# Performance work log

Measured on AMD Instinct MI355X. Metric: run time of the kernel, lower is better.

Reference implementation:

```python
import jax, jax.numpy as jnp
import numpy as np

B, L, H, N2, NLAYERS = 8, 4096, 256, 32, 4


def setup_inputs() -> dict:
    key = jax.random.key(0)
    ks = jax.random.split(key, 7)
    x = jax.random.normal(ks[0], (B, L, H), dtype=jnp.float32)
    # S4D kernel params (per layer, stacked on leading dim)
    dt_min, dt_max = 1e-3, 1e-1
    u = jax.random.uniform(ks[1], (NLAYERS, H), dtype=jnp.float32)
    log_dt = u * (np.log(dt_max) - np.log(dt_min)) + np.log(dt_min)
    log_A_real = jnp.log(0.5 * jnp.ones((NLAYERS, H, N2), jnp.float32))
    A_imag = jnp.broadcast_to(np.pi * jnp.arange(N2, dtype=jnp.float32), (NLAYERS, H, N2)) * jnp.ones((NLAYERS, H, N2), jnp.float32)
    C_re = jax.random.normal(ks[2], (NLAYERS, H, N2), dtype=jnp.float32) * (0.5 ** 0.5)
    C_im = jax.random.normal(ks[3], (NLAYERS, H, N2), dtype=jnp.float32) * (0.5 ** 0.5)
    D = jax.random.normal(ks[4], (NLAYERS, H), dtype=jnp.float32)
    Wout = jax.random.normal(ks[5], (NLAYERS, 2 * H, H), dtype=jnp.float32) * (1.0 / H) ** 0.5
    bout = jnp.zeros((NLAYERS, 2 * H), jnp.float32)
    ln_g = jnp.ones((NLAYERS, H), jnp.float32)
    ln_b = jnp.zeros((NLAYERS, H), jnp.float32)
    return dict(x=x, log_dt=log_dt, log_A_real=log_A_real, A_imag=A_imag,
                C_re=C_re, C_im=C_im, D=D, Wout=Wout, bout=bout,
                ln_g=ln_g, ln_b=ln_b)


def _s4d_kernel(log_dt, log_A_real, A_imag, C_re, C_im, Lseq):
    # Vandermonde kernel of S4D: k[h,l] = 2*Re sum_n C'_hn exp(dt_h*A_hn*l)
    dt = jnp.exp(log_dt)                       # (H,)
    A = (-jnp.exp(log_A_real) + 1j * A_imag)   # (H,N) complex
    C = C_re + 1j * C_im                       # (H,N)
    dtA = A * dt[:, None]                      # (H,N)
    K = jnp.exp(dtA[:, :, None] * jnp.arange(Lseq, dtype=jnp.float32))  # (H,N,L)
    Cm = C * (jnp.exp(dtA) - 1.0) / A          # ZOH discretization of C
    return 2.0 * jnp.einsum('hn,hnl->hl', Cm, K).real  # (H,L)


def _s4d_layer(u, log_dt, log_A_real, A_imag, C_re, C_im, D, Wout, bout):
    # u: (B,H,L)
    Lq = u.shape[-1]
    k = _s4d_kernel(log_dt, log_A_real, A_imag, C_re, C_im, Lq)  # (H,L)
    kf = jnp.fft.rfft(k, n=2 * Lq)             # (H, L+1)
    uf = jnp.fft.rfft(u, n=2 * Lq)             # (B,H,L+1)
    y = jnp.fft.irfft(uf * kf, n=2 * Lq)[..., :Lq]
    y = y + u * D[:, None]
    y = jax.nn.gelu(y, approximate=False)
    # output linear: 1x1 conv H->2H followed by GLU along channel dim
    y = jnp.einsum('oh,bhl->bol', Wout, y) + bout[None, :, None]
    a, b = jnp.split(y, 2, axis=1)
    return a * jax.nn.sigmoid(b)               # (B,H,L)


def _layernorm_ch(x, g, b, eps=1e-5):
    # x: (B,H,L); normalize over channel axis H (matches norm on (B,L,H))
    m = jnp.mean(x, axis=1, keepdims=True)
    v = jnp.mean((x - m) ** 2, axis=1, keepdims=True)
    return (x - m) / jnp.sqrt(v + eps) * g[None, :, None] + b[None, :, None]


def reference(x, log_dt, log_A_real, A_imag, C_re, C_im, D, Wout, bout, ln_g, ln_b):
    u = jnp.swapaxes(x, -1, -2)  # (B,H,L)
    for i in range(NLAYERS):  # post-norm (prenorm=False), dropout=identity (eval)
        z = _s4d_layer(u, log_dt[i], log_A_real[i], A_imag[i], C_re[i], C_im[i],
                       D[i], Wout[i], bout[i])
        u = z + u
        u = _layernorm_ch(u, ln_g[i], ln_b[i])
    return jnp.swapaxes(u, -1, -2)  # (B,L,H)
```

## Files before the change

### kernel.cpp

```cpp
#include <hip/hip_runtime.h>
#include <math.h>

#define B    8
#define L    4096
#define H    256
#define N2   32
#define NL   4
#define O2   512
#define BLK  64
#define NBLK 64
#define TVP  136
#define MJP  72
#define UTP  72
#define INP  66
#define TL2  64
#define YPAD 264

typedef __attribute__((ext_vector_type(8))) short short8;
typedef __attribute__((ext_vector_type(4))) float f32x4;

__device__ __forceinline__ unsigned short f2bf(float f)
{
    unsigned int u = __float_as_uint(f);
    unsigned int r = (u + 0x7fffu + ((u >> 16) & 1u)) >> 16;
    return (unsigned short)r;
}

__device__ __forceinline__ float bf2f(unsigned short v)
{
    return __uint_as_float(((unsigned int)v) << 16);
}

__device__ __forceinline__ float gelu_f(float x)
{
    float t = 1.59576912161f * fmaf(0.044715f * x * x, x, x);
    return x / (1.f + __expf(-t));
}

__global__ __launch_bounds__(64) void k_mats(
    const float* __restrict__ log_dt, const float* __restrict__ log_Ar,
    const float* __restrict__ A_im, const float* __restrict__ C_re,
    const float* __restrict__ C_im, const float* __restrict__ Dv,
    unsigned short* __restrict__ TVc, unsigned short* __restrict__ Mm,
    float2* __restrict__ w64c)
{
    __shared__ float kb[2][BLK];
    const int t = threadIdx.x;
    const int g = t >> 5, n = t & 31;
    const int id = blockIdx.x * 2 + g;
    const int layer = id >> 8, h = id & 255;
    const int idx = (layer * H + h) * N2 + n;
    double dt = exp((double)log_dt[layer * H + h]);
    double Ar = -exp((double)log_Ar[idx]);
    double Ai = (double)A_im[idx];
    double dtr = dt * Ar, dti = dt * Ai;
    double er = exp(dtr);
    double dwr = er * cos(dti), dwi = er * sin(dti);
    double numr = dwr - 1.0, numi = dwi;
    double den = Ar * Ar + Ai * Ai;
    double qr0 = (numr * Ar + numi * Ai) / den;
    double qi0 = (numi * Ar - numr * Ai) / den;
    double dcr = (double)C_re[idx], dci = (double)C_im[idx];
    const float wr = (float)dwr, wi = (float)dwi;
    const float cr = (float)(2.0 * (dcr * qr0 - dci * qi0));
    const float ci = (float)(2.0 * (dcr * qi0 + dci * qr0));
    const float Dh = Dv[layer * H + h];
    unsigned short* tv = TVc + (size_t)(layer * H + h) * BLK * TVP;
    unsigned short* mm = Mm + (size_t)(layer * H + h) * BLK * MJP;
    float vr = 1.f, vi = 0.f;
    for (int d = 0; d < BLK; ++d) {
        float pk = fmaf(cr, vr, -(ci * vi));
        pk += __shfl_xor(pk, 1);  pk += __shfl_xor(pk, 2);
        pk += __shfl_xor(pk, 4);  pk += __shfl_xor(pk, 8);
        pk += __shfl_xor(pk, 16);
        if (n == 0) kb[g][d] = pk;
        mm[n * MJP + (63 - d)]        = f2bf(vr);
        mm[(32 + n) * MJP + (63 - d)] = f2bf(vi);
        float nvr = vr * wr - vi * wi;
        float nvi = vr * wi + vi * wr;
        vr = nvr; vi = nvi;
        float qr = fmaf(cr, vr, -(ci * vi));
        float qi = fmaf(cr, vi, ci * vr);
        tv[d * TVP + 64 + n] = f2bf(qr);
        tv[d * TVP + 96 + n] = f2bf(-qi);
    }
    w64c[(layer * H + h) * N2 + n] = make_float2(vr, vi);
    __syncthreads();
    for (int i = 0; i < BLK; ++i) {
#pragma unroll
        for (int hf = 0; hf < 2; ++hf) {
            int j = n + hf * 32;
            float val = (j > i) ? 0.f : ((j == i) ? (kb[g][0] + Dh) : kb[g][i - j]);
            tv[i * TVP + j] = f2bf(val);
        }
    }
}

__global__ __launch_bounds__(256) void k_tr_xu(const float* __restrict__ x, unsigned short* __restrict__ u)
{
    __shared__ float t[32][33];
    int b = blockIdx.z;
    int h0 = blockIdx.x * 32, l0 = blockIdx.y * 32;
    int tx = threadIdx.x & 31, ty = threadIdx.x >> 5;
    const float* xb = x + (size_t)b * L * H;
    unsigned short* ub = u + (size_t)b * H * L;
#pragma unroll
    for (int i = 0; i < 4; ++i)
        t[ty + i * 8][tx] = xb[(size_t)(l0 + ty + i * 8) * H + h0 + tx];
    __syncthreads();
#pragma unroll
    for (int i = 0; i < 4; ++i)
        ub[(size_t)(h0 + ty + i * 8) * L + l0 + tx] = f2bf(t[tx][ty + i * 8]);
}

__global__ __launch_bounds__(256) void k_wcvt(const float* __restrict__ w, unsigned short* __restrict__ wb)
{
    int idx = (blockIdx.x * 256 + threadIdx.x) * 4;
    float4 v = *(const float4*)(w + idx);
    ushort4 o;
    o.x = f2bf(v.x); o.y = f2bf(v.y); o.z = f2bf(v.z); o.w = f2bf(v.w);
    *(ushort4*)(wb + idx) = o;
}

__global__ __launch_bounds__(256) void k_scan3(
    const unsigned short* __restrict__ u, const unsigned short* __restrict__ Mm_l,
    const unsigned short* __restrict__ TVc_l, const float2* __restrict__ w64c_l,
    unsigned short* __restrict__ y)
{
    __shared__ __align__(16) unsigned short uT[BLK * UTP];
    __shared__ __align__(16) unsigned short ST[BLK * UTP];
    __shared__ float INC[BLK * INP];
    __shared__ float2 cLd[4][32];
    const int t = threadIdx.x;
    const int wv = t >> 6, lane = t & 63;
    const int lanei = lane & 15, quad = lane >> 4;
    const int h = blockIdx.x >> 3, ct = blockIdx.x & 7;
    const unsigned short* ub = u + (size_t)(ct * H + h) * L;

    {
        int col = t >> 2, q = t & 3;
        *(short8*)&uT[col * UTP + q * 16]     = *(const short8*)(ub + col * 64 + q * 16);
        *(short8*)&uT[col * UTP + q * 16 + 8] = *(const short8*)(ub + col * 64 + q * 16 + 8);
    }
    __syncthreads();

    {
        f32x4 acc[4];
#pragma unroll
        for (int nt = 0; nt < 4; ++nt) acc[nt] = (f32x4){0.f, 0.f, 0.f, 0.f};
        const unsigned short* arow = Mm_l + (size_t)h * BLK * MJP + (wv * 16 + lanei) * MJP + quad * 8;
#pragma unroll
        for (int kt = 0; kt < 2; ++kt) {
            short8 a8 = *(const short8*)(arow + kt * 32);
#pragma unroll
            for (int nt = 0; nt < 4; ++nt) {
                short8 b8 = *(const short8*)&uT[(nt * 16 + lanei) * UTP + kt * 32 + quad * 8];
                acc[nt] = __builtin_amdgcn_mfma_f32_16x16x32_bf16(a8, b8, acc[nt], 0, 0, 0);
            }
        }
#pragma unroll
        for (int nt = 0; nt < 4; ++nt) {
            int col = nt * 16 + lanei;
            int k0 = wv * 16 + quad * 4;
#pragma unroll
            for (int reg = 0; reg < 4; ++reg)
                INC[col * INP + k0 + reg] = acc[nt][reg];
        }
    }
    __syncthreads();

    {
        const int n = lane & 31;
        float Pr[16], Pi[16];
        float w1r = 1.f, w1i = 0.f;
        float2 w64 = make_float2(0.f, 0.f);
        if (lane < 32) {
            w64 = w64c_l[h * N2 + n];
            float sr = 0.f, si = 0.f;
            const int base = wv * 16;
#pragma unroll
            for (int k = 0; k < 16; ++k) {
                Pr[k] = sr; Pi[k] = si;
                float ir = INC[(base + k) * INP + n];
                float ii = INC[(base + k) * INP + 32 + n];
                float nr = fmaf(w64.x, sr, fmaf(-w64.y, si, ir));
                float ni = fmaf(w64.x, si, fmaf(w64.y, sr, ii));
                sr = nr; si = ni;
            }
            cLd[wv][n] = make_float2(sr, si);
            float ar = w64.x, ai = w64.y;
#pragma unroll
            for (int q = 0; q < 4; ++q) {
                float nr2 = ar * ar - ai * ai;
                float ni2 = 2.f * ar * ai;
                ar = nr2; ai = ni2;
            }
            w1r = ar; w1i = ai;
        }
        __syncthreads();
        if (lane < 32) {
            float Cr = 0.f, Ci = 0.f;
            for (int wp = 0; wp < wv; ++wp) {
                float2 Lw = cLd[wp][n];
                float nr = fmaf(w1r, Cr, fmaf(-w1i, Ci, Lw.x));
                float ni = fmaf(w1r, Ci, fmaf(w1i, Cr, Lw.y));
                Cr = nr; Ci = ni;
            }
            float pr = 1.f, pi = 0.f;
#pragma unroll
            for (int k = 0; k < 16; ++k) {
                int blk = wv * 16 + k;
                float Sr = fmaf(pr, Cr, fmaf(-pi, Ci, Pr[k]));
                float Si = fmaf(pr, Ci, fmaf(pi, Cr, Pi[k]));
                ST[blk * UTP + n]      = f2bf(Sr);
                ST[blk * UTP + 32 + n] = f2bf(Si);
                float npr = pr * w64.x - pi * w64.y;
                float npi = pr * w64.y + pi * w64.x;
                pr = npr; pi = npi;
            }
        }
    }
    __syncthreads();

    {
        f32x4 acc[4];
#pragma unroll
        for (int nt = 0; nt < 4; ++nt) acc[nt] = (f32x4){0.f, 0.f, 0.f, 0.f};
        const unsigned short* arow = TVc_l + (size_t)h * BLK * TVP + (wv * 16 + lanei) * TVP + quad * 8;
#pragma unroll
        for (int kt = 0; kt < 4; ++kt) {
            short8 a8 = *(const short8*)(arow + kt * 32);
            const unsigned short* bb = (kt < 2) ? uT : ST;
            int ko = (kt & 1) * 32 + quad * 8;
#pragma unroll
            for (int nt = 0; nt < 4; ++nt) {
                short8 b8 = *(const short8*)&bb[(nt * 16 + lanei) * UTP + ko];
                acc[nt] = __builtin_amdgcn_mfma_f32_16x16x32_bf16(a8, b8, acc[nt], 0, 0, 0);
            }
        }
        unsigned short* yb = y + (size_t)(ct * H + h) * L;
#pragma unroll
        for (int nt = 0; nt < 4; ++nt) {
            int blk = nt * 16 + lanei;
            int i0 = wv * 16 + quad * 4;
            ushort4 o4;
            o4.x = f2bf(gelu_f(acc[nt][0]));
            o4.y = f2bf(gelu_f(acc[nt][1]));
            o4.z = f2bf(gelu_f(acc[nt][2]));
            o4.w = f2bf(gelu_f(acc[nt][3]));
            *(ushort4*)(yb + blk * 64 + i0) = o4;
        }
    }
}

__global__ __launch_bounds__(512, 4) void k_gemm(
    const unsigned short* __restrict__ y, unsigned short* __restrict__ u,
    const unsigned short* __restrict__ Wb, const float* __restrict__ bo,
    const float* __restrict__ lng, const float* __restrict__ lnb,
    float* __restrict__ outp)
{
    __shared__ __align__(16) unsigned short yS[TL2 * YPAD];
    __shared__ float bS[O2];
    __shared__ float lgS[H], lbS[H];
    __shared__ float redS[8][4][16], redQ[8][4][16];

    const int t = threadIdx.x;
    const int wv = t >> 6;
    const int lane = t & 63;
    const int lanei = lane & 15;
    const int quad = lane >> 4;
    const int b = blockIdx.x >> 6;
    const int l0 = (blockIdx.x & 63) * TL2;

    {
        const int i = t & 7, hr = t >> 3;
        const unsigned short* yb = y + (size_t)b * H * L + l0 + i * 8;
#pragma unroll
        for (int ps = 0; ps < 4; ++ps) {
            int h = ps * 64 + hr;
            short8 v8 = *(const short8*)(yb + (size_t)h * L);
#pragma unroll
            for (int r = 0; r < 8; ++r)
                yS[(i * 8 + r) * YPAD + (h ^ (8 * i))] = (unsigned short)v8[r];
        }
        if (t < O2) bS[t] = bo[t];
        if (t < H) { lgS[t] = lng[t]; lbS[t] = lnb[t]; }
    }
    __syncthreads();

    f32x4 acc[2][2][4];
#pragma unroll
    for (int p = 0; p < 2; ++p)
#pragma unroll
        for (int jj = 0; jj < 2; ++jj)
#pragma unroll
            for (int nt = 0; nt < 4; ++nt)
                acc[p][jj][nt] = (f32x4){0.f, 0.f, 0.f, 0.f};

    size_t abase[2][2];
#pragma unroll
    for (int p = 0; p < 2; ++p)
#pragma unroll
        for (int jj = 0; jj < 2; ++jj)
            abase[p][jj] = (size_t)(p * 256 + wv * 32 + jj * 16 + lanei) * H + quad * 8;

#pragma unroll
    for (int kt = 0; kt < 8; ++kt) {
        short8 bfr[4];
#pragma unroll
        for (int nt = 0; nt < 4; ++nt) {
            int lp = nt * 16 + lanei;
            int a = (2 * nt + (lanei >> 3)) & 7;
            bfr[nt] = *(const short8*)&yS[lp * YPAD + ((kt * 32 + quad * 8) ^ (8 * a))];
        }
#pragma unroll
        for (int p = 0; p < 2; ++p)
#pragma unroll
            for (int jj = 0; jj < 2; ++jj) {
                short8 a8 = *(const short8*)(Wb + abase[p][jj] + kt * 32);
#pragma unroll
                for (int nt = 0; nt < 4; ++nt)
                    acc[p][jj][nt] = __builtin_amdgcn_mfma_f32_16x16x32_bf16(
                        a8, bfr[nt], acc[p][jj][nt], 0, 0, 0);
            }
    }

    float psum[4] = {0.f, 0.f, 0.f, 0.f}, psq[4] = {0.f, 0.f, 0.f, 0.f};
    unsigned short* ub = u + (size_t)b * H * L + l0;
#pragma unroll
    for (int jj = 0; jj < 2; ++jj) {
#pragma unroll
        for (int nt = 0; nt < 4; ++nt) {
            int lc = nt * 16 + lanei;
#pragma unroll
            for (int reg = 0; reg < 4; ++reg) {
                int o = wv * 32 + jj * 16 + quad * 4 + reg;
                float a = acc[0][jj][nt][reg] + bS[o];
                float g = acc[1][jj][nt][reg] + bS[o + 256];
                float glu = a / (1.f + __expf(-g));
                float val = glu + bf2f(ub[(size_t)o * L + lc]);
                acc[0][jj][nt][reg] = val;
                psum[nt] += val;
                psq[nt] = fmaf(val, val, psq[nt]);
            }
        }
    }
#pragma unroll
    for (int nt = 0; nt < 4; ++nt) {
        psum[nt] += __shfl_xor(psum[nt], 16);
        psum[nt] += __shfl_xor(psum[nt], 32);
        psq[nt]  += __shfl_xor(psq[nt], 16);
        psq[nt]  += __shfl_xor(psq[nt], 32);
    }
    if (lane < 16) {
#pragma unroll
        for (int nt = 0; nt < 4; ++nt) {
            redS[wv][nt][lanei] = psum[nt];
            redQ[wv][nt][lanei] = psq[nt];
        }
    }
    __syncthreads();
    float mcol[4], icol[4];
#pragma unroll
    for (int nt = 0; nt < 4; ++nt) {
        float s = 0.f, q = 0.f;
#pragma unroll
        for (int w = 0; w < 8; ++w) { s += redS[w][nt][lanei]; q += redQ[w][nt][lanei]; }
        float m = s * (1.0f / 256.0f);
        float v = q * (1.0f / 256.0f) - m * m;
        mcol[nt] = m;
        icol[nt] = rsqrtf(v + 1e-5f);
    }
    if (outp == nullptr) {
#pragma unroll
        for (int jj = 0; jj < 2; ++jj) {
#pragma unroll
            for (int nt = 0; nt < 4; ++nt) {
                int lc = nt * 16 + lanei;
#pragma unroll
                for (int reg = 0; reg < 4; ++reg) {
                    int o = wv * 32 + jj * 16 + quad * 4 + reg;
                    float val = acc[0][jj][nt][reg];
                    float ov = (val - mcol[nt]) * icol[nt] * lgS[o] + lbS[o];
                    ub[(size_t)o * L + lc] = f2bf(ov);
                }
            }
        }
    } else {
#pragma unroll
        for (int jj = 0; jj < 2; ++jj) {
#pragma unroll
            for (int nt = 0; nt < 4; ++nt) {
                int lc = nt * 16 + lanei;
                int o0 = wv * 32 + jj * 16 + quad * 4;
                float4 ov;
#pragma unroll
                for (int reg = 0; reg < 4; ++reg) {
                    int o = o0 + reg;
                    float val = acc[0][jj][nt][reg];
                    ((float*)&ov)[reg] = (val - mcol[nt]) * icol[nt] * lgS[o] + lbS[o];
                }
                *(float4*)(outp + ((size_t)b * L + l0 + lc) * H + o0) = ov;
            }
        }
    }
}

extern "C" void kernel_launch(void* const* d_in, const int* in_sizes, int n_in,
                              void* d_out, int out_size, void* d_ws, size_t ws_size,
                              hipStream_t stream)
{
    const float* x      = (const float*)d_in[0];
    const float* log_dt = (const float*)d_in[1];
    const float* log_Ar = (const float*)d_in[2];
    const float* A_im   = (const float*)d_in[3];
    const float* C_re   = (const float*)d_in[4];
    const float* C_im   = (const float*)d_in[5];
    const float* Dv     = (const float*)d_in[6];
    const float* Wout   = (const float*)d_in[7];
    const float* bout   = (const float*)d_in[8];
    const float* lng    = (const float*)d_in[9];
    const float* lnb    = (const float*)d_in[10];
    float* out = (float*)d_out;

    unsigned short* u   = (unsigned short*)d_ws;
    unsigned short* Wb  = u + (size_t)B * H * L;
    unsigned short* TVc = Wb + (size_t)NL * O2 * H;
    unsigned short* Mm  = TVc + (size_t)NL * H * BLK * TVP;
    float2* w64c        = (float2*)(Mm + (size_t)NL * H * BLK * MJP);
    unsigned short* y   = (unsigned short*)(w64c + (size_t)NL * H * N2);

    k_wcvt<<<NL * O2 * H / 1024, 256, 0, stream>>>(Wout, Wb);
    k_mats<<<NL * H / 2, 64, 0, stream>>>(log_dt, log_Ar, A_im, C_re, C_im, Dv, TVc, Mm, w64c);
    k_tr_xu<<<dim3(8, 128, B), 256, 0, stream>>>(x, u);
    for (int layer = 0; layer < NL; ++layer) {
        k_scan3<<<H * 8, 256, 0, stream>>>(u, Mm + (size_t)layer * H * BLK * MJP,
                                           TVc + (size_t)layer * H * BLK * TVP,
                                           w64c + (size_t)layer * H * N2, y);
        k_gemm<<<B * L / TL2, 512, 0, stream>>>(y, u, Wb + (size_t)layer * O2 * H,
                                                bout + layer * O2, lng + layer * H, lnb + layer * H,
                                                (layer == NL - 1) ? out : nullptr);
    }
}
```

Baseline: 321.4 us.

## Swap scan MFMA operands to drop barriers, merge setup kernels, prefetch GEMM weights

In k_scan3 the MFMA operands are swapped so each wave produces and consumes only its own 16 block rows. This lets the INC stores become 16-byte vector writes and removes two block-wide __syncthreads, since the scan and the second GEMM now read only data written by the same wave. The three setup kernels (weight conversion, S4D matrix construction, x transpose) are merged into one launch with block-index dispatch, which cuts launch overhead and the k_mats occupancy to 256 threads per block. k_gemm also loads the first K-slice of Wout fragments before filling the LDS tile, to overlap that global latency. The INC padding changes to 68 so the rows stay 16-byte aligned for the vector stores.

```diff
diff --git a/kernel.cpp b/kernel.cpp
--- a/kernel.cpp
+++ b/kernel.cpp
@@ -12,7 +12,7 @@
 #define TVP  136
 #define MJP  72
 #define UTP  72
-#define INP  66
+#define INP  68
 #define TL2  64
 #define YPAD 264
 
@@ -37,89 +37,91 @@
     return x / (1.f + __expf(-t));
 }
 
-__global__ __launch_bounds__(64) void k_mats(
-    const float* __restrict__ log_dt, const float* __restrict__ log_Ar,
-    const float* __restrict__ A_im, const float* __restrict__ C_re,
-    const float* __restrict__ C_im, const float* __restrict__ Dv,
-    unsigned short* __restrict__ TVc, unsigned short* __restrict__ Mm,
-    float2* __restrict__ w64c)
-{
-    __shared__ float kb[2][BLK];
+__global__ __launch_bounds__(256) void k_setup(
+    const float* __restrict__ x, const float* __restrict__ log_dt,
+    const float* __restrict__ log_Ar, const float* __restrict__ A_im,
+    const float* __restrict__ C_re, const float* __restrict__ C_im,
+    const float* __restrict__ Dv, const float* __restrict__ Wout,
+    unsigned short* __restrict__ Wb, unsigned short* __restrict__ TVc,
+    unsigned short* __restrict__ Mm, float2* __restrict__ w64c,
+    unsigned short* __restrict__ u)
+{
+    __shared__ float sh[32 * 33];
+    const int bid = blockIdx.x;
     const int t = threadIdx.x;
-    const int g = t >> 5, n = t & 31;
-    const int id = blockIdx.x * 2 + g;
-    const int layer = id >> 8, h = id & 255;
-    const int idx = (layer * H + h) * N2 + n;
-    double dt = exp((double)log_dt[layer * H + h]);
-    double Ar = -exp((double)log_Ar[idx]);
-    double Ai = (double)A_im[idx];
-    double dtr = dt * Ar, dti = dt * Ai;
-    double er = exp(dtr);
-    double dwr = er * cos(dti), dwi = er * sin(dti);
-    double numr = dwr - 1.0, numi = dwi;
-    double den = Ar * Ar + Ai * Ai;
-    double qr0 = (numr * Ar + numi * Ai) / den;
-    double qi0 = (numi * Ar - numr * Ai) / den;
-    double dcr = (double)C_re[idx], dci = (double)C_im[idx];
-    const float wr = (float)dwr, wi = (float)dwi;
-    const float cr = (float)(2.0 * (dcr * qr0 - dci * qi0));
-    const float ci = (float)(2.0 * (dcr * qi0 + dci * qr0));
-    const float Dh = Dv[layer * H + h];
-    unsigned short* tv = TVc + (size_t)(layer * H + h) * BLK * TVP;
-    unsigned short* mm = Mm + (size_t)(layer * H + h) * BLK * MJP;
-    float vr = 1.f, vi = 0.f;
-    for (int d = 0; d < BLK; ++d) {
-        float pk = fmaf(cr, vr, -(ci * vi));
-        pk += __shfl_xor(pk, 1);  pk += __shfl_xor(pk, 2);
-        pk += __shfl_xor(pk, 4);  pk += __shfl_xor(pk, 8);
-        pk += __shfl_xor(pk, 16);
-        if (n == 0) kb[g][d] = pk;
-        mm[n * MJP + (63 - d)]        = f2bf(vr);
-        mm[(32 + n) * MJP + (63 - d)] = f2bf(vi);
-        float nvr = vr * wr - vi * wi;
-        float nvi = vr * wi + vi * wr;
-        vr = nvr; vi = nvi;
-        float qr = fmaf(cr, vr, -(ci * vi));
-        float qi = fmaf(cr, vi, ci * vr);
-        tv[d * TVP + 64 + n] = f2bf(qr);
-        tv[d * TVP + 96 + n] = f2bf(-qi);
-    }
-    w64c[(layer * H + h) * N2 + n] = make_float2(vr, vi);
-    __syncthreads();
-    for (int i = 0; i < BLK; ++i) {
-#pragma unroll
-        for (int hf = 0; hf < 2; ++hf) {
-            int j = n + hf * 32;
-            float val = (j > i) ? 0.f : ((j == i) ? (kb[g][0] + Dh) : kb[g][i - j]);
-            tv[i * TVP + j] = f2bf(val);
-        }
-    }
-}
-
-__global__ __launch_bounds__(256) void k_tr_xu(const float* __restrict__ x, unsigned short* __restrict__ u)
-{
-    __shared__ float t[32][33];
-    int b = blockIdx.z;
-    int h0 = blockIdx.x * 32, l0 = blockIdx.y * 32;
-    int tx = threadIdx.x & 31, ty = threadIdx.x >> 5;
-    const float* xb = x + (size_t)b * L * H;
-    unsigned short* ub = u + (size_t)b * H * L;
-#pragma unroll
-    for (int i = 0; i < 4; ++i)
-        t[ty + i * 8][tx] = xb[(size_t)(l0 + ty + i * 8) * H + h0 + tx];
-    __syncthreads();
-#pragma unroll
-    for (int i = 0; i < 4; ++i)
-        ub[(size_t)(h0 + ty + i * 8) * L + l0 + tx] = f2bf(t[tx][ty + i * 8]);
-}
-
-__global__ __launch_bounds__(256) void k_wcvt(const float* __restrict__ w, unsigned short* __restrict__ wb)
-{
-    int idx = (blockIdx.x * 256 + threadIdx.x) * 4;
-    float4 v = *(const float4*)(w + idx);
-    ushort4 o;
-    o.x = f2bf(v.x); o.y = f2bf(v.y); o.z = f2bf(v.z); o.w = f2bf(v.w);
-    *(ushort4*)(wb + idx) = o;
+
+    if (bid < 512) {
+        int idx = (bid * 256 + t) * 4;
+        float4 v = *(const float4*)(Wout + idx);
+        ushort4 o;
+        o.x = f2bf(v.x); o.y = f2bf(v.y); o.z = f2bf(v.z); o.w = f2bf(v.w);
+        *(ushort4*)(Wb + idx) = o;
+    } else if (bid < 640) {
+        float* kb = sh;
+        const int g = t >> 5, n = t & 31;
+        const int id = (bid - 512) * 8 + g;
+        const int layer = id >> 8, h = id & 255;
+        const int idx = (layer * H + h) * N2 + n;
+        double dt = exp((double)log_dt[layer * H + h]);
+        double Ar = -exp((double)log_Ar[idx]);
+        double Ai = (double)A_im[idx];
+        double dtr = dt * Ar, dti = dt * Ai;
+        double er = exp(dtr);
+        double dwr = er * cos(dti), dwi = er * sin(dti);
+        double numr = dwr - 1.0, numi = dwi;
+        double den = Ar * Ar + Ai * Ai;
+        double qr0 = (numr * Ar + numi * Ai) / den;
+        double qi0 = (numi * Ar - numr * Ai) / den;
+        double dcr = (double)C_re[idx], dci = (double)C_im[idx];
+        const float wr = (float)dwr, wi = (float)dwi;
+        const float cr = (float)(2.0 * (dcr * qr0 - dci * qi0));
+        const float ci = (float)(2.0 * (dcr * qi0 + dci * qr0));
+        const float Dh = Dv[layer * H + h];
+        unsigned short* tv = TVc + (size_t)(layer * H + h) * BLK * TVP;
+        unsigned short* mm = Mm + (size_t)(layer * H + h) * BLK * MJP;
+        float vr = 1.f, vi = 0.f;
+        for (int d = 0; d < BLK; ++d) {
+            float pk = fmaf(cr, vr, -(ci * vi));
+            pk += __shfl_xor(pk, 1);  pk += __shfl_xor(pk, 2);
+            pk += __shfl_xor(pk, 4);  pk += __shfl_xor(pk, 8);
+            pk += __shfl_xor(pk, 16);
+            if (n == 0) kb[g * 64 + d] = pk;
+            mm[n * MJP + (63 - d)]        = f2bf(vr);
+            mm[(32 + n) * MJP + (63 - d)] = f2bf(vi);
+            float nvr = vr * wr - vi * wi;
+            float nvi = vr * wi + vi * wr;
+            vr = nvr; vi = nvi;
+            float qr = fmaf(cr, vr, -(ci * vi));
+            float qi = fmaf(cr, vi, ci * vr);
+            tv[d * TVP + 64 + n] = f2bf(qr);
+            tv[d * TVP + 96 + n] = f2bf(-qi);
+        }
+        w64c[(layer * H + h) * N2 + n] = make_float2(vr, vi);
+        __syncthreads();
+        for (int i = 0; i < BLK; ++i) {
+#pragma unroll
+            for (int hf = 0; hf < 2; ++hf) {
+                int j = n + hf * 32;
+                float val = (j > i) ? 0.f : ((j == i) ? (kb[g * 64] + Dh) : kb[g * 64 + i - j]);
+                tv[i * TVP + j] = f2bf(val);
+            }
+        }
+    } else {
+        float (*tt)[33] = (float(*)[33])sh;
+        const int rb = bid - 640;
+        const int hx = rb & 7, ly = (rb >> 3) & 127, b = rb >> 10;
+        const int h0 = hx * 32, l0 = ly * 32;
+        const int tx = t & 31, ty = t >> 5;
+        const float* xb = x + (size_t)b * L * H;
+        unsigned short* ub = u + (size_t)b * H * L;
+#pragma unroll
+        for (int i = 0; i < 4; ++i)
+            tt[ty + i * 8][tx] = xb[(size_t)(l0 + ty + i * 8) * H + h0 + tx];
+        __syncthreads();
+#pragma unroll
+        for (int i = 0; i < 4; ++i)
+            ub[(size_t)(h0 + ty + i * 8) * L + l0 + tx] = f2bf(tt[tx][ty + i * 8]);
+    }
 }
 
 __global__ __launch_bounds__(256) void k_scan3(
@@ -129,7 +131,7 @@
 {
     __shared__ __align__(16) unsigned short uT[BLK * UTP];
     __shared__ __align__(16) unsigned short ST[BLK * UTP];
-    __shared__ float INC[BLK * INP];
+    __shared__ __align__(16) float INC[BLK * INP];
     __shared__ float2 cLd[4][32];
     const int t = threadIdx.x;
     const int wv = t >> 6, lane = t & 63;
@@ -148,101 +150,92 @@
         f32x4 acc[4];
 #pragma unroll
         for (int nt = 0; nt < 4; ++nt) acc[nt] = (f32x4){0.f, 0.f, 0.f, 0.f};
-        const unsigned short* arow = Mm_l + (size_t)h * BLK * MJP + (wv * 16 + lanei) * MJP + quad * 8;
+        const unsigned short* bcol = &uT[(wv * 16 + lanei) * UTP + quad * 8];
+        const unsigned short* abase = Mm_l + (size_t)h * BLK * MJP + lanei * MJP + quad * 8;
 #pragma unroll
         for (int kt = 0; kt < 2; ++kt) {
-            short8 a8 = *(const short8*)(arow + kt * 32);
+            short8 b8 = *(const short8*)(bcol + kt * 32);
 #pragma unroll
             for (int nt = 0; nt < 4; ++nt) {
-                short8 b8 = *(const short8*)&uT[(nt * 16 + lanei) * UTP + kt * 32 + quad * 8];
+                short8 a8 = *(const short8*)(abase + (nt * 16) * MJP + kt * 32);
                 acc[nt] = __builtin_amdgcn_mfma_f32_16x16x32_bf16(a8, b8, acc[nt], 0, 0, 0);
             }
         }
 #pragma unroll
-        for (int nt = 0; nt < 4; ++nt) {
-            int col = nt * 16 + lanei;
-            int k0 = wv * 16 + quad * 4;
-#pragma unroll
-            for (int reg = 0; reg < 4; ++reg)
-                INC[col * INP + k0 + reg] = acc[nt][reg];
-        }
+        for (int nt = 0; nt < 4; ++nt)
+            *(f32x4*)&INC[(wv * 16 + lanei) * INP + nt * 16 + quad * 4] = acc[nt];
+    }
+
+    const int n = lane & 31;
+    float Pr[16], Pi[16];
+    float w1r = 1.f, w1i = 0.f;
+    float2 w64 = make_float2(0.f, 0.f);
+    if (lane < 32) {
+        w64 = w64c_l[h * N2 + n];
+        float sr = 0.f, si = 0.f;
+        const int base = wv * 16;
+#pragma unroll
+        for (int k = 0; k < 16; ++k) {
+            Pr[k] = sr; Pi[k] = si;
+            float ir = INC[(base + k) * INP + n];
+            float ii = INC[(base + k) * INP + 32 + n];
+            float nr = fmaf(w64.x, sr, fmaf(-w64.y, si, ir));
+            float ni = fmaf(w64.x, si, fmaf(w64.y, sr, ii));
+            sr = nr; si = ni;
+        }
+        cLd[wv][n] = make_float2(sr, si);
+        float ar = w64.x, ai = w64.y;
+#pragma unroll
+        for (int q = 0; q < 4; ++q) {
+            float nr2 = ar * ar - ai * ai;
+            float ni2 = 2.f * ar * ai;
+            ar = nr2; ai = ni2;
+        }
+        w1r = ar; w1i = ai;
     }
     __syncthreads();
-
-    {
-        const int n = lane & 31;
-        float Pr[16], Pi[16];
-        float w1r = 1.f, w1i = 0.f;
-        float2 w64 = make_float2(0.f, 0.f);
-        if (lane < 32) {
-            w64 = w64c_l[h * N2 + n];
-            float sr = 0.f, si = 0.f;
-            const int base = wv * 16;
-#pragma unroll
-            for (int k = 0; k < 16; ++k) {
-                Pr[k] = sr; Pi[k] = si;
-                float ir = INC[(base + k) * INP + n];
-                float ii = INC[(base + k) * INP + 32 + n];
-                float nr = fmaf(w64.x, sr, fmaf(-w64.y, si, ir));
-                float ni = fmaf(w64.x, si, fmaf(w64.y, sr, ii));
-                sr = nr; si = ni;
-            }
-            cLd[wv][n] = make_float2(sr, si);
-            float ar = w64.x, ai = w64.y;
-#pragma unroll
-            for (int q = 0; q < 4; ++q) {
-                float nr2 = ar * ar - ai * ai;
-                float ni2 = 2.f * ar * ai;
-                ar = nr2; ai = ni2;
-            }
-            w1r = ar; w1i = ai;
-        }
-        __syncthreads();
-        if (lane < 32) {
-            float Cr = 0.f, Ci = 0.f;
-            for (int wp = 0; wp < wv; ++wp) {
-                float2 Lw = cLd[wp][n];
-                float nr = fmaf(w1r, Cr, fmaf(-w1i, Ci, Lw.x));
-                float ni = fmaf(w1r, Ci, fmaf(w1i, Cr, Lw.y));
-                Cr = nr; Ci = ni;
-            }
-            float pr = 1.f, pi = 0.f;
-#pragma unroll
-            for (int k = 0; k < 16; ++k) {
-                int blk = wv * 16 + k;
-                float Sr = fmaf(pr, Cr, fmaf(-pi, Ci, Pr[k]));
-                float Si = fmaf(pr, Ci, fmaf(pi, Cr, Pi[k]));
-                ST[blk * UTP + n]      = f2bf(Sr);
-                ST[blk * UTP + 32 + n] = f2bf(Si);
-                float npr = pr * w64.x - pi * w64.y;
-                float npi = pr * w64.y + pi * w64.x;
-                pr = npr; pi = npi;
-            }
-        }
-    }
-    __syncthreads();
+    if (lane < 32) {
+        float Cr = 0.f, Ci = 0.f;
+        for (int wp = 0; wp < wv; ++wp) {
+            float2 Lw = cLd[wp][n];
+            float nr = fmaf(w1r, Cr, fmaf(-w1i, Ci, Lw.x));
+            float ni = fmaf(w1r, Ci, fmaf(w1i, Cr, Lw.y));
+            Cr = nr; Ci = ni;
+        }
+        float pr = 1.f, pi = 0.f;
+#pragma unroll
+        for (int k = 0; k < 16; ++k) {
+            int blk = wv * 16 + k;
+            float Sr = fmaf(pr, Cr, fmaf(-pi, Ci, Pr[k]));
+            float Si = fmaf(pr, Ci, fmaf(pi, Cr, Pi[k]));
+            ST[blk * UTP + n]      = f2bf(Sr);
+            ST[blk * UTP + 32 + n] = f2bf(Si);
+            float npr = pr * w64.x - pi * w64.y;
+            float npi = pr * w64.y + pi * w64.x;
+            pr = npr; pi = npi;
+        }
+    }
 
     {
         f32x4 acc[4];
 #pragma unroll
         for (int nt = 0; nt < 4; ++nt) acc[nt] = (f32x4){0.f, 0.f, 0.f, 0.f};
-        const unsigned short* arow = TVc_l + (size_t)h * BLK * TVP + (wv * 16 + lanei) * TVP + quad * 8;
+        const unsigned short* abase = TVc_l + (size_t)h * BLK * TVP + lanei * TVP + quad * 8;
 #pragma unroll
         for (int kt = 0; kt < 4; ++kt) {
-            short8 a8 = *(const short8*)(arow + kt * 32);
             const unsigned short* bb = (kt < 2) ? uT : ST;
-            int ko = (kt & 1) * 32 + quad * 8;
+            short8 b8 = *(const short8*)&bb[(wv * 16 + lanei) * UTP + (kt & 1) * 32 + quad * 8];
 #pragma unroll
             for (int nt = 0; nt < 4; ++nt) {
-                short8 b8 = *(const short8*)&bb[(nt * 16 + lanei) * UTP + ko];
+                short8 a8 = *(const short8*)(abase + (nt * 16) * TVP + kt * 32);
                 acc[nt] = __builtin_amdgcn_mfma_f32_16x16x32_bf16(a8, b8, acc[nt], 0, 0, 0);
             }
         }
         unsigned short* yb = y + (size_t)(ct * H + h) * L;
 #pragma unroll
         for (int nt = 0; nt < 4; ++nt) {
-            int blk = nt * 16 + lanei;
-            int i0 = wv * 16 + quad * 4;
+            int blk = wv * 16 + lanei;
+            int i0 = nt * 16 + quad * 4;
             ushort4 o4;
             o4.x = f2bf(gelu_f(acc[nt][0]));
             o4.y = f2bf(gelu_f(acc[nt][1]));
@@ -272,6 +265,20 @@
     const int b = blockIdx.x >> 6;
     const int l0 = (blockIdx.x & 63) * TL2;
 
+    size_t abase[2][2];
+#pragma unroll
+    for (int p = 0; p < 2; ++p)
+#pragma unroll
+        for (int jj = 0; jj < 2; ++jj)
+            abase[p][jj] = (size_t)(p * 256 + wv * 32 + jj * 16 + lanei) * H + quad * 8;
+
+    short8 a8p[4];
+#pragma unroll
+    for (int p = 0; p < 2; ++p)
+#pragma unroll
+        for (int jj = 0; jj < 2; ++jj)
+            a8p[p * 2 + jj] = *(const short8*)(Wb + abase[p][jj]);
+
     {
         const int i = t & 7, hr = t >> 3;
         const unsigned short* yb = y + (size_t)b * H * L + l0 + i * 8;
@@ -296,13 +303,6 @@
 #pragma unroll
             for (int nt = 0; nt < 4; ++nt)
                 acc[p][jj][nt] = (f32x4){0.f, 0.f, 0.f, 0.f};
-
-    size_t abase[2][2];
-#pragma unroll
-    for (int p = 0; p < 2; ++p)
-#pragma unroll
-        for (int jj = 0; jj < 2; ++jj)
-            abase[p][jj] = (size_t)(p * 256 + wv * 32 + jj * 16 + lanei) * H + quad * 8;
 
 #pragma unroll
     for (int kt = 0; kt < 8; ++kt) {
@@ -317,7 +317,8 @@
         for (int p = 0; p < 2; ++p)
 #pragma unroll
             for (int jj = 0; jj < 2; ++jj) {
-                short8 a8 = *(const short8*)(Wb + abase[p][jj] + kt * 32);
+                short8 a8 = (kt == 0) ? a8p[p * 2 + jj]
+                                      : *(const short8*)(Wb + abase[p][jj] + kt * 32);
 #pragma unroll
                 for (int nt = 0; nt < 4; ++nt)
                     acc[p][jj][nt] = __builtin_amdgcn_mfma_f32_16x16x32_bf16(
@@ -430,9 +431,8 @@
     float2* w64c        = (float2*)(Mm + (size_t)NL * H * BLK * MJP);
     unsigned short* y   = (unsigned short*)(w64c + (size_t)NL * H * N2);
 
-    k_wcvt<<<NL * O2 * H / 1024, 256, 0, stream>>>(Wout, Wb);
-    k_mats<<<NL * H / 2, 64, 0, stream>>>(log_dt, log_Ar, A_im, C_re, C_im, Dv, TVc, Mm, w64c);
-    k_tr_xu<<<dim3(8, 128, B), 256, 0, stream>>>(x, u);
+    k_setup<<<8832, 256, 0, stream>>>(x, log_dt, log_Ar, A_im, C_re, C_im, Dv, Wout,
+                                      Wb, TVc, Mm, w64c, u);
     for (int layer = 0; layer < NL; ++layer) {
         k_scan3<<<H * 8, 256, 0, stream>>>(u, Mm + (size_t)layer * H * BLK * MJP,
                                            TVc + (size_t)layer * H * BLK * TVP,
```

Result: no change. 326.4 us (+1.6%).
